# Performance work log

Hardware: AMD Instinct MI355X
Metric: run time of the kernel (lower is better)

Reference implementation:

```python
import jax, jax.numpy as jnp
import numpy as np

D = 1024; NH = 16; HD = 64; FF = 4096; DEPTH = 4
P = 14; C = 3; GRID = 32; MERGE = 2; NIMG = 4
L = GRID * GRID; S = NIMG * L; ORIG = 24; EPS = 1e-6
SCALE = HD ** -0.5


def setup_inputs() -> dict:
    key = jax.random.key(0)
    ks = jax.random.split(key, 12)
    s = 0.02
    return {
        "pixel_values": jax.random.normal(ks[0], (S, C * P * P), jnp.float32),
        "grid_thw": jnp.tile(jnp.array([[1, GRID, GRID]], jnp.int32), (NIMG, 1)),
        "conv_w": jax.random.normal(ks[1], (D, C * P * P), jnp.float32) * s,
        "conv_b": jnp.zeros((D,), jnp.float32),
        "pos_embed": jax.random.normal(ks[2], (ORIG * ORIG, D), jnp.float32) * s,
        "ln1_g": jnp.ones((DEPTH, D), jnp.float32),
        "ln1_b": jnp.zeros((DEPTH, D), jnp.float32),
        "qkv_w": jax.random.normal(ks[3], (DEPTH, 3 * D, D), jnp.float32) * s,
        "qkv_b": jnp.zeros((DEPTH, 3 * D), jnp.float32),
        "proj_w": jax.random.normal(ks[4], (DEPTH, D, D), jnp.float32) * s,
        "proj_b": jnp.zeros((DEPTH, D), jnp.float32),
        "ln2_g": jnp.ones((DEPTH, D), jnp.float32),
        "ln2_b": jnp.zeros((DEPTH, D), jnp.float32),
        "fc1_w": jax.random.normal(ks[5], (DEPTH, FF, D), jnp.float32) * s,
        "fc1_b": jnp.zeros((DEPTH, FF), jnp.float32),
        "fc2_w": jax.random.normal(ks[6], (DEPTH, D, FF), jnp.float32) * s,
        "fc2_b": jnp.zeros((DEPTH, D), jnp.float32),
    }


def _pos_ids():
    # rot_pos_emb spatial-merge permutation for one t=1 image, tiled over images
    h = jnp.broadcast_to(jnp.arange(GRID)[:, None], (GRID, GRID))
    w = jnp.broadcast_to(jnp.arange(GRID)[None, :], (GRID, GRID))
    def perm(a):
        a = a.reshape(GRID // MERGE, MERGE, GRID // MERGE, MERGE)
        return a.transpose(0, 2, 1, 3).reshape(-1)
    hpos = jnp.tile(perm(h), NIMG)  # [S]
    wpos = jnp.tile(perm(w), NIMG)
    return hpos, wpos


def _bilinear_border(img, nx, ny):
    # img [H, W, D]; nx, ny in [-1, 1]; align_corners=False, padding_mode='border'
    Hh, Ww, _ = img.shape
    x = (nx + 1.0) * 0.5 * Ww - 0.5
    y = (ny + 1.0) * 0.5 * Hh - 0.5
    x0 = jnp.floor(x); y0 = jnp.floor(y)
    wx = (x - x0)[:, None]; wy = (y - y0)[:, None]
    x0i = jnp.clip(x0.astype(jnp.int32), 0, Ww - 1)
    x1i = jnp.clip(x0.astype(jnp.int32) + 1, 0, Ww - 1)
    y0i = jnp.clip(y0.astype(jnp.int32), 0, Hh - 1)
    y1i = jnp.clip(y0.astype(jnp.int32) + 1, 0, Hh - 1)
    v00 = img[y0i, x0i]; v01 = img[y0i, x1i]
    v10 = img[y1i, x0i]; v11 = img[y1i, x1i]
    return (v00 * (1 - wy) * (1 - wx) + v01 * (1 - wy) * wx
            + v10 * wy * (1 - wx) + v11 * wy * wx)


def _ln(x, g, b):
    m = jnp.mean(x, axis=-1, keepdims=True)
    v = jnp.mean(jnp.square(x - m), axis=-1, keepdims=True)
    return (x - m) * jax.lax.rsqrt(v + EPS) * g + b


def _forward(pixel_values, conv_w, conv_b, pos_embed, ln1_g, ln1_b, qkv_w, qkv_b,
             proj_w, proj_b, ln2_g, ln2_b, fc1_w, fc1_b, fc2_w, fc2_b):
    # patch embed: conv with kernel==stride==patch over one patch == linear
    x = pixel_values @ conv_w.T + conv_b  # [S, D]

    # interpolated 2D position embedding (grid_sample bilinear, border pad)
    hpos, wpos = _pos_ids()
    norm_w = (wpos.astype(jnp.float32) + 0.5) / GRID * 2.0 - 1.0
    norm_h = (hpos.astype(jnp.float32) + 0.5) / GRID * 2.0 - 1.0
    pe = _bilinear_border(pos_embed.reshape(ORIG, ORIG, D), norm_w, norm_h)
    x = x + pe

    for i in range(DEPTH):
        # attention (block-diagonal over equal-length images -> batched)
        r = x
        y = _ln(x, ln1_g[i], ln1_b[i])
        qkv = (y @ qkv_w[i].T + qkv_b[i]).reshape(NIMG, L, 3, NH, HD)
        q = qkv[:, :, 0].transpose(0, 2, 1, 3)  # [B, H, L, hd]
        k = qkv[:, :, 1].transpose(0, 2, 1, 3)
        v = qkv[:, :, 2].transpose(0, 2, 1, 3)
        scores = jnp.einsum('bhqd,bhkd->bhqk', q, k) * SCALE
        probs = jax.nn.softmax(scores, axis=-1)
        o = jnp.einsum('bhqk,bhkd->bhqd', probs, v)
        o = o.transpose(0, 2, 1, 3).reshape(S, D)
        x = r + o @ proj_w[i].T + proj_b[i]
        # MLP
        r = x
        y = _ln(x, ln2_g[i], ln2_b[i])
        h = jax.nn.gelu(y @ fc1_w[i].T + fc1_b[i], approximate=False)
        x = r + h @ fc2_w[i].T + fc2_b[i]
    return x


def reference(pixel_values, grid_thw, conv_w, conv_b, pos_embed, ln1_g, ln1_b,
              qkv_w, qkv_b, proj_w, proj_b, ln2_g, ln2_b, fc1_w, fc1_b, fc2_w, fc2_b):
    return _forward(pixel_values, conv_w, conv_b, pos_embed, ln1_g, ln1_b, qkv_w,
                    qkv_b, proj_w, proj_b, ln2_g, ln2_b, fc1_w, fc1_b, fc2_w, fc2_b)
```

## Files before the change

kernel.cpp:

```cpp
#include <hip/hip_runtime.h>
#include <math.h>

typedef __bf16 bf16x8 __attribute__((ext_vector_type(8)));
typedef float f32x4 __attribute__((ext_vector_type(4)));
typedef short s16x4 __attribute__((ext_vector_type(4)));
typedef short s16x8 __attribute__((ext_vector_type(8)));

static __device__ __forceinline__ short f2bs(float f) {
  return __builtin_bit_cast(short, (__bf16)f);
}

#define GLL16(gp, lp) __builtin_amdgcn_global_load_lds( \
    (const __attribute__((address_space(1))) void*)(gp), \
    (__attribute__((address_space(3))) void*)(lp), 16, 0, 0)

__global__ __launch_bounds__(256) void cvt_f32_bf16(const float* __restrict__ s,
                                                    short* __restrict__ d, int n) {
  int stride = gridDim.x * blockDim.x * 4;
  for (int j = (blockIdx.x * blockDim.x + threadIdx.x) * 4; j < n; j += stride) {
    float4 v = *(const float4*)(s + j);
    s16x4 o;
    o[0] = f2bs(v.x); o[1] = f2bs(v.y); o[2] = f2bs(v.z); o[3] = f2bs(v.w);
    *(s16x4*)(d + j) = o;
  }
}

__global__ __launch_bounds__(256) void cvt_pad(const float* __restrict__ s,
                                               short* __restrict__ d) {
  int r = blockIdx.x;
  for (int c = threadIdx.x; c < 608; c += blockDim.x)
    d[(size_t)r * 608 + c] = (c < 588) ? f2bs(s[(size_t)r * 588 + c]) : (short)0;
}

template <int N, int K, int EPI, int CM, int CN>
__global__ __launch_bounds__(256) void gemm_bt(const short* __restrict__ A,
                                               const short* __restrict__ B,
                                               const float* __restrict__ bias,
                                               const float* __restrict__ resid,
                                               void* __restrict__ out) {
  static_assert(K % 32 == 0, "K");
  constexpr int NT = K / 32;
  static_assert(NT >= 3, "pipeline depth");
  constexpr int NX = N / 128, NY = 32;
  constexpr int nwg = NX * NY;
  static_assert(nwg % 8 == 0 && (nwg / 8) % (CM * CN) == 0, "chunk");
  static_assert(NX % CN == 0 && NY % CM == 0, "cells");
  __shared__ short lA[3][128 * 32];
  __shared__ short lB[3][128 * 32];

  const int o = blockIdx.x;
  const int wid = (o & 7) * (nwg / 8) + (o >> 3);
  constexpr int cellsz = CM * CN;
  const int cell = wid / cellsz, within = wid % cellsz;
  constexpr int cellsx = NX / CN;
  const int bm0 = ((cell / cellsx) * CM + within / CN) * 128;
  const int bn0 = ((cell % cellsx) * CN + within % CN) * 128;

  const int t = threadIdx.x, w = t >> 6, lane = t & 63;
  const int wr = w >> 1, wc = w & 1;
  f32x4 acc[4][4] = {};

  const int srow = t >> 2;
  const int scol = ((t & 3) ^ ((srow >> 1) & 3)) * 8;
  const short* aP = A + (size_t)(bm0 + srow) * K + scol;
  const short* bP = B + (size_t)(bn0 + srow) * K + scol;
  const int sdst0 = (w * 16) * 32;
  const int sdst1 = (64 + w * 16) * 32;

  const int lr = lane & 15;
  const int qx = ((lane >> 4) ^ ((lr >> 1) & 3)) * 8;

  auto stage = [&](int buf, int ko) {
    GLL16(aP + ko, &lA[buf][sdst0]);
    GLL16(aP + ko + (size_t)64 * K, &lA[buf][sdst1]);
    GLL16(bP + ko, &lB[buf][sdst0]);
    GLL16(bP + ko + (size_t)64 * K, &lB[buf][sdst1]);
  };

  stage(0, 0);
  stage(1, 32);
  stage(2, 64);

  int buf = 0;
  for (int kt = 0; kt < NT; ++kt) {
    if (kt < NT - 2)       asm volatile("s_waitcnt vmcnt(8)" ::: "memory");
    else if (kt == NT - 2) asm volatile("s_waitcnt vmcnt(4)" ::: "memory");
    else                   asm volatile("s_waitcnt vmcnt(0)" ::: "memory");
    __builtin_amdgcn_s_barrier();
    asm volatile("" ::: "memory");
    __builtin_amdgcn_sched_barrier(0);

    bf16x8 af[4], bg[4];
#pragma unroll
    for (int mi = 0; mi < 4; ++mi)
      af[mi] = *(const bf16x8*)&lA[buf][(wr * 64 + mi * 16 + lr) * 32 + qx];
#pragma unroll
    for (int ni = 0; ni < 4; ++ni)
      bg[ni] = *(const bf16x8*)&lB[buf][(wc * 64 + ni * 16 + lr) * 32 + qx];

    asm volatile("s_waitcnt lgkmcnt(0)" ::: "memory");
    __builtin_amdgcn_sched_barrier(0);
    __builtin_amdgcn_s_barrier();
    asm volatile("" ::: "memory");
    __builtin_amdgcn_sched_barrier(0);

    if (kt + 3 < NT) stage(buf, (kt + 3) * 32);
    __builtin_amdgcn_sched_barrier(0);

#pragma unroll
    for (int mi = 0; mi < 4; ++mi)
#pragma unroll
      for (int ni = 0; ni < 4; ++ni)
        acc[mi][ni] = __builtin_amdgcn_mfma_f32_16x16x32_bf16(af[mi], bg[ni],
                                                              acc[mi][ni], 0, 0, 0);
    buf = (buf == 2) ? 0 : buf + 1;
  }

  const int lg4 = (lane >> 4) * 4;
#pragma unroll
  for (int mi = 0; mi < 4; ++mi) {
#pragma unroll
    for (int ni = 0; ni < 4; ++ni) {
      const int row = bm0 + wr * 64 + mi * 16 + lg4;
      const int col = bn0 + wc * 64 + ni * 16 + lr;
      const float bc = bias[col];
#pragma unroll
      for (int r = 0; r < 4; ++r) {
        float v = acc[mi][ni][r] + bc;
        size_t idx = (size_t)(row + r) * N + col;
        if constexpr (EPI == 1) v = 0.5f * v * (1.0f + erff(v * 0.70710678118f));
        if constexpr (EPI == 0 || EPI == 1) ((short*)out)[idx] = f2bs(v);
        else if constexpr (EPI == 2) ((float*)out)[idx] = v + resid[idx];
        else ((float*)out)[idx] = v;
      }
    }
  }
}

template <int N, int KC, int LDK, int EPI, int CM, int CN, int KSPLIT>
__global__ __launch_bounds__(512, 2) void gemm256(const short* __restrict__ A,
                                                  const short* __restrict__ B,
                                                  const float* __restrict__ bias,
                                                  void* __restrict__ out) {
  static_assert(KC % 64 == 0, "K");
  constexpr int NKT = KC / 64;
  static_assert(NKT >= 3 && (NKT % 2) == 0, "ktiles");
  constexpr int NXT = N / 256, MYT = 16;
  constexpr int nwg = NXT * MYT * KSPLIT;
  constexpr int cellsz = CM * CN;
  static_assert(nwg % 8 == 0 && (nwg / 8) % cellsz == 0, "chunk");
  static_assert((NXT * MYT) % cellsz == 0, "cellspace");
  static_assert(NXT % CN == 0 && MYT % CM == 0, "cells");

  __shared__ short sA[2][2][8192];
  __shared__ short sB[2][2][8192];

  const int o = blockIdx.x;
  const int wid = (o & 7) * (nwg / 8) + (o >> 3);
  const int kc = wid / (NXT * MYT);
  const int rem = wid % (NXT * MYT);
  const int cell = rem / cellsz, within = rem % cellsz;
  constexpr int cellsx = NXT / CN;
  const int bm0 = ((cell / cellsx) * CM + within / CN) * 256;
  const int bn0 = ((cell % cellsx) * CN + within % CN) * 256;

  const int tid = threadIdx.x, wv = tid >> 6, lane = tid & 63;
  const int wrow = wv >> 2, wcol = wv & 3;
  const int lr = lane & 15, lg = lane >> 4;

  const int sr0 = tid >> 2;
  const int sc0 = ((tid & 3) ^ ((sr0 >> 1) & 3)) * 8;
  const short* aS0 = A + (size_t)(bm0 + sr0) * LDK + kc * KC + sc0;
  const short* bS0 = B + (size_t)(bn0 + sr0) * LDK + kc * KC + sc0;
  const int ld0 = wv * 512, ld1 = 4096 + wv * 512;

  auto stageA = [&](int d, int h, int kt) {
    const int off = kt * 64 + h * 32;
    GLL16(aS0 + off, &sA[d][h][ld0]);
    GLL16(aS0 + off + (size_t)128 * LDK, &sA[d][h][ld1]);
  };
  auto stageB = [&](int d, int h, int kt) {
    const int off = kt * 64 + h * 32;
    GLL16(bS0 + off, &sB[d][h][ld0]);
    GLL16(bS0 + off + (size_t)128 * LDK, &sB[d][h][ld1]);
  };

  const int chR = (lg ^ ((lr >> 1) & 3)) * 8;
  const int rA0 = wrow * 128 + lr;
  const int rB0 = wcol * 64 + lr;

  f32x4 acc[8][4] = {};

  stageA(0, 0, 0); stageB(0, 0, 0);
  stageA(0, 1, 0); stageB(0, 1, 0);
  stageA(1, 0, 1); stageB(1, 0, 1);
  asm volatile("s_waitcnt vmcnt(8)" ::: "memory");
  __builtin_amdgcn_sched_barrier(0);
  __builtin_amdgcn_s_barrier();

  bf16x8 af[4], bf[4];

#define LDA(mh, ks, d)                                                        \
  _Pragma("unroll")                                                           \
  for (int f = 0; f < 4; ++f)                                                 \
    af[f] = *(const bf16x8*)&sA[d][ks][(rA0 + (mh)*64 + f * 16) * 32 + chR];
#define LDB(ks, d)                                                            \
  _Pragma("unroll")                                                           \
  for (int n = 0; n < 4; ++n)                                                 \
    bf[n] = *(const bf16x8*)&sB[d][ks][(rB0 + n * 16) * 32 + chR];
#define MFMA16(mh)                                                            \
  __builtin_amdgcn_s_setprio(1);                                              \
  _Pragma("unroll")                                                           \
  for (int f = 0; f < 4; ++f)                                                 \
    _Pragma("unroll")                                                         \
    for (int n = 0; n < 4; ++n)                                               \
      acc[(mh)*4 + f][n] = __builtin_amdgcn_mfma_f32_16x16x32_bf16(           \
          af[f], bf[n], acc[(mh)*4 + f][n], 0, 0, 0);                         \
  __builtin_amdgcn_s_setprio(0);
#define PH_BAR1                                                               \
  __builtin_amdgcn_s_barrier();                                               \
  asm volatile("s_waitcnt lgkmcnt(0)" ::: "memory");                          \
  __builtin_amdgcn_sched_barrier(0);
#define PH_END                                                                \
  __builtin_amdgcn_s_barrier();
#define PH_END_V                                                              \
  asm volatile("s_waitcnt vmcnt(8)" ::: "memory");                            \
  __builtin_amdgcn_sched_barrier(0);                                          \
  __builtin_amdgcn_s_barrier();

  for (int t = 0; t < NKT; ++t) {
    const int d = t & 1;
    int t1 = t + 1; if (t1 >= NKT) t1 -= NKT;
    int t2 = t + 2; if (t2 >= NKT) t2 -= NKT;
    const int d1 = t1 & 1, d2 = t2 & 1;

    LDA(0, 0, d); LDB(0, d);
    stageA(d1, 1, t1);
    PH_BAR1; MFMA16(0); PH_END;
    LDA(1, 0, d);
    stageB(d1, 1, t1);
    PH_BAR1; MFMA16(1); PH_END_V;
    LDA(0, 1, d); LDB(1, d);
    stageA(d2, 0, t2);
    PH_BAR1; MFMA16(0); PH_END;
    LDA(1, 1, d);
    stageB(d2, 0, t2);
    PH_BAR1; MFMA16(1); PH_END_V;
  }
#undef LDA
#undef LDB
#undef MFMA16
#undef PH_BAR1
#undef PH_END
#undef PH_END_V

  const int lg4 = lg * 4;
#pragma unroll
  for (int mh = 0; mh < 2; ++mh) {
#pragma unroll
    for (int f = 0; f < 4; ++f) {
#pragma unroll
      for (int n = 0; n < 4; ++n) {
        const int row = bm0 + wrow * 128 + mh * 64 + f * 16 + lg4;
        const int col = bn0 + wcol * 64 + n * 16 + lr;
        float bc = 0.f;
        if constexpr (EPI != 5) bc = bias[col];
#pragma unroll
        for (int r = 0; r < 4; ++r) {
          float v = acc[mh * 4 + f][n][r] + bc;
          if constexpr (EPI == 1) v = 0.5f * v * (1.0f + erff(v * 0.70710678118f));
          if constexpr (EPI == 5)
            ((float*)out)[((size_t)kc << 22) + (size_t)(row + r) * N + col] = v;
          else
            ((short*)out)[(size_t)(row + r) * N + col] = f2bs(v);
        }
      }
    }
  }
}

__global__ __launch_bounds__(256) void fc2_reduce(const float* __restrict__ part,
                                                  const float* __restrict__ bias,
                                                  const float* __restrict__ resid,
                                                  float* __restrict__ dest) {
  const size_t i4 = ((size_t)blockIdx.x * 256 + threadIdx.x) * 4;
  const float4 a0 = *(const float4*)(part + i4);
  const float4 a1 = *(const float4*)(part + (1ull << 22) + i4);
  const float4 a2 = *(const float4*)(part + (2ull << 22) + i4);
  const float4 a3 = *(const float4*)(part + (3ull << 22) + i4);
  const float4 rv = *(const float4*)(resid + i4);
  const float4 bv = *(const float4*)(bias + (i4 & 1023));
  float4 o;
  o.x = a0.x + a1.x + a2.x + a3.x + rv.x + bv.x;
  o.y = a0.y + a1.y + a2.y + a3.y + rv.y + bv.y;
  o.z = a0.z + a1.z + a2.z + a3.z + rv.z + bv.z;
  o.w = a0.w + a1.w + a2.w + a3.w + rv.w + bv.w;
  *(float4*)(dest + i4) = o;
}

__global__ __launch_bounds__(256) void ln_fwd(const float* __restrict__ x,
                                              const float* __restrict__ g,
                                              const float* __restrict__ b,
                                              short* __restrict__ y) {
  const int row = blockIdx.x, t = threadIdx.x, w = t >> 6, lane = t & 63;
  const float4 v = ((const float4*)(x + (size_t)row * 1024))[t];
  float s = v.x + v.y + v.z + v.w;
  float ss = v.x * v.x + v.y * v.y + v.z * v.z + v.w * v.w;
#pragma unroll
  for (int m = 1; m < 64; m <<= 1) { s += __shfl_xor(s, m); ss += __shfl_xor(ss, m); }
  __shared__ float rs[4], rss[4];
  if (lane == 0) { rs[w] = s; rss[w] = ss; }
  __syncthreads();
  s = rs[0] + rs[1] + rs[2] + rs[3];
  ss = rss[0] + rss[1] + rss[2] + rss[3];
  const float mean = s * (1.f / 1024.f);
  const float var = ss * (1.f / 1024.f) - mean * mean;
  const float rstd = rsqrtf(var + 1e-6f);
  const float4 gv = ((const float4*)g)[t];
  const float4 bv = ((const float4*)b)[t];
  s16x4 o;
  o[0] = f2bs((v.x - mean) * rstd * gv.x + bv.x);
  o[1] = f2bs((v.y - mean) * rstd * gv.y + bv.y);
  o[2] = f2bs((v.z - mean) * rstd * gv.z + bv.z);
  o[3] = f2bs((v.w - mean) * rstd * gv.w + bv.w);
  *(s16x4*)(y + (size_t)row * 1024 + t * 4) = o;
}

__global__ __launch_bounds__(256) void pos_add(float* __restrict__ x,
                                               const float* __restrict__ pe) {
  const int sidx = blockIdx.x;
  const int f = sidx & 1023;
  const int wq = 2 * ((f >> 2) & 15) + (f & 1);
  const int hq = 2 * (f >> 6) + ((f >> 1) & 1);
  const float gx = (wq + 0.5f) * 0.75f - 0.5f;
  const float gy = (hq + 0.5f) * 0.75f - 0.5f;
  const float fx = floorf(gx), fy = floorf(gy);
  const float wx = gx - fx, wy = gy - fy;
  int x0 = (int)fx, y0 = (int)fy;
  const int x0i = x0 < 0 ? 0 : (x0 > 23 ? 23 : x0);
  const int x1i = (x0 + 1) < 0 ? 0 : ((x0 + 1) > 23 ? 23 : x0 + 1);
  const int y0i = y0 < 0 ? 0 : (y0 > 23 ? 23 : y0);
  const int y1i = (y0 + 1) < 0 ? 0 : ((y0 + 1) > 23 ? 23 : y0 + 1);
  const float w00 = (1 - wy) * (1 - wx), w01 = (1 - wy) * wx;
  const float w10 = wy * (1 - wx), w11 = wy * wx;
  const int c = threadIdx.x * 4;
  const float4 p00 = *(const float4*)(pe + (size_t)(y0i * 24 + x0i) * 1024 + c);
  const float4 p01 = *(const float4*)(pe + (size_t)(y0i * 24 + x1i) * 1024 + c);
  const float4 p10 = *(const float4*)(pe + (size_t)(y1i * 24 + x0i) * 1024 + c);
  const float4 p11 = *(const float4*)(pe + (size_t)(y1i * 24 + x1i) * 1024 + c);
  float* xp = x + (size_t)sidx * 1024 + c;
  float4 xv = *(float4*)xp;
  xv.x += w00 * p00.x + w01 * p01.x + w10 * p10.x + w11 * p11.x;
  xv.y += w00 * p00.y + w01 * p01.y + w10 * p10.y + w11 * p11.y;
  xv.z += w00 * p00.z + w01 * p01.z + w10 * p10.z + w11 * p11.z;
  xv.w += w00 * p00.w + w01 * p01.w + w10 * p10.w + w11 * p11.w;
  *(float4*)xp = xv;
}

__global__ __launch_bounds__(256) void attn_fwd(const short* __restrict__ qkv,
                                                short* __restrict__ outp) {
  __shared__ short lK[2][64 * 64];
  __shared__ short Vt[2][64 * 72];
  const int t = threadIdx.x, w = t >> 6, lane = t & 63;
  const int b = blockIdx.y >> 4, h = blockIdx.y & 15;
  const int sbase = b * 1024;
  const int q0 = blockIdx.x * 64 + w * 16;
  const int lr = lane & 15, lg = lane >> 4;

  const short* qrow = qkv + (size_t)(sbase + q0 + lr) * 3072 + h * 64;
  const bf16x8 qf0 = *(const bf16x8*)(qrow + lg * 8);
  const bf16x8 qf1 = *(const bf16x8*)(qrow + 32 + lg * 8);

  const int krofs = t >> 3;
  const int kcol = ((t & 7) ^ (krofs & 7)) * 8;
  const short* ksrc = qkv + (size_t)(sbase + krofs) * 3072 + 1024 + h * 64 + kcol;
  const int vkv = t >> 2, vdp = t & 3;
  const short* vsrc = qkv + (size_t)(sbase + vkv) * 3072 + 2048 + h * 64 + vdp * 16;
  const int vph = vkv ^ (vdp << 4);

  f32x4 o[4] = {};
  float mrun = -1e30f, lsum = 0.f;

  s16x8 v0 = *(const s16x8*)vsrc;
  s16x8 v1 = *(const s16x8*)(vsrc + 8);
  GLL16(ksrc, &lK[0][(w * 8) * 64]);
  GLL16(ksrc + (size_t)32 * 3072, &lK[0][(32 + w * 8) * 64]);
#pragma unroll
  for (int j = 0; j < 8; ++j) Vt[0][(vdp * 16 + j) * 72 + vph] = v0[j];
#pragma unroll
  for (int j = 0; j < 8; ++j) Vt[0][(vdp * 16 + 8 + j) * 72 + vph] = v1[j];
  asm volatile("s_waitcnt vmcnt(0) lgkmcnt(0)" ::: "memory");
  __builtin_amdgcn_s_barrier();

  int buf = 0;
  for (int kb = 0; kb < 16; ++kb) {
    if (kb < 15) {
      const short* vs = vsrc + (size_t)(kb + 1) * 64 * 3072;
      v0 = *(const s16x8*)vs;
      v1 = *(const s16x8*)(vs + 8);
      const short* ks = ksrc + (size_t)(kb + 1) * 64 * 3072;
      GLL16(ks, &lK[buf ^ 1][(w * 8) * 64]);
      GLL16(ks + (size_t)32 * 3072, &lK[buf ^ 1][(32 + w * 8) * 64]);
    }

    f32x4 s[4];
    __builtin_amdgcn_s_setprio(1);
#pragma unroll
    for (int sub = 0; sub < 4; ++sub) {
      const int krow = (sub * 16 + lr) * 64;
      const bf16x8 kf0 = *(const bf16x8*)&lK[buf][krow + (lg ^ (lr & 7)) * 8];
      const bf16x8 kf1 = *(const bf16x8*)&lK[buf][krow + ((lg + 4) ^ (lr & 7)) * 8];
      f32x4 a = {};
      a = __builtin_amdgcn_mfma_f32_16x16x32_bf16(kf0, qf0, a, 0, 0, 0);
      a = __builtin_amdgcn_mfma_f32_16x16x32_bf16(kf1, qf1, a, 0, 0, 0);
      s[sub] = a;
    }
    __builtin_amdgcn_s_setprio(0);

    constexpr float SC = 0.125f * 1.44269504089f;
    float sl[16];
#pragma unroll
    for (int sub = 0; sub < 4; ++sub)
#pragma unroll
      for (int r = 0; r < 4; ++r) sl[sub * 4 + r] = s[sub][r] * SC;
    float tm = sl[0];
#pragma unroll
    for (int i = 1; i < 16; ++i) tm = fmaxf(tm, sl[i]);
    tm = fmaxf(tm, __shfl_xor(tm, 16));
    tm = fmaxf(tm, __shfl_xor(tm, 32));
    if (!__all(tm <= mrun + 12.0f)) {
      const float newm = fmaxf(mrun, tm);
      const float sc = exp2f(mrun - newm);
      lsum *= sc;
#pragma unroll
      for (int f = 0; f < 4; ++f) {
        o[f][0] *= sc; o[f][1] *= sc; o[f][2] *= sc; o[f][3] *= sc;
      }
      mrun = newm;
    }
    s16x4 pb[4];
    float psum = 0.f;
#pragma unroll
    for (int sub = 0; sub < 4; ++sub)
#pragma unroll
      for (int r = 0; r < 4; ++r) {
        const float p = exp2f(sl[sub * 4 + r] - mrun);
        psum += p;
        pb[sub][r] = f2bs(p);
      }
    psum += __shfl_xor(psum, 16);
    psum += __shfl_xor(psum, 32);
    lsum += psum;

    __builtin_amdgcn_s_setprio(1);
#pragma unroll
    for (int f = 0; f < 4; ++f) {
      const int vrow = (f * 16 + lr) * 72;
#pragma unroll
      for (int sub = 0; sub < 4; ++sub) {
        const s16x4 va = *(const s16x4*)&Vt[buf][vrow + ((sub ^ f) << 4) + lg * 4];
        o[f] = __builtin_amdgcn_mfma_f32_16x16x16bf16_1k(va, pb[sub], o[f], 0, 0, 0);
      }
    }
    __builtin_amdgcn_s_setprio(0);

    if (kb < 15) {
#pragma unroll
      for (int j = 0; j < 8; ++j) Vt[buf ^ 1][(vdp * 16 + j) * 72 + vph] = v0[j];
#pragma unroll
      for (int j = 0; j < 8; ++j) Vt[buf ^ 1][(vdp * 16 + 8 + j) * 72 + vph] = v1[j];
      asm volatile("s_waitcnt vmcnt(0) lgkmcnt(0)" ::: "memory");
      __builtin_amdgcn_s_barrier();
      buf ^= 1;
    }
  }

  const float inv = 1.0f / lsum;
  short* orow = outp + (size_t)(sbase + q0 + lr) * 1024 + h * 64;
#pragma unroll
  for (int f = 0; f < 4; ++f) {
    s16x4 ov;
    ov[0] = f2bs(o[f][0] * inv); ov[1] = f2bs(o[f][1] * inv);
    ov[2] = f2bs(o[f][2] * inv); ov[3] = f2bs(o[f][3] * inv);
    *(s16x4*)(orow + f * 16 + lg * 4) = ov;
  }
}

extern "C" void kernel_launch(void* const* d_in, const int* in_sizes, int n_in,
                              void* d_out, int out_size, void* d_ws, size_t ws_size,
                              hipStream_t stream) {
  const float* pixel  = (const float*)d_in[0];
  const float* conv_w = (const float*)d_in[2];
  const float* conv_b = (const float*)d_in[3];
  const float* pos_e  = (const float*)d_in[4];
  const float* ln1_g  = (const float*)d_in[5];
  const float* ln1_b  = (const float*)d_in[6];
  const float* qkv_w  = (const float*)d_in[7];
  const float* qkv_b  = (const float*)d_in[8];
  const float* proj_w = (const float*)d_in[9];
  const float* proj_b = (const float*)d_in[10];
  const float* ln2_g  = (const float*)d_in[11];
  const float* ln2_b  = (const float*)d_in[12];
  const float* fc1_w  = (const float*)d_in[13];
  const float* fc1_b  = (const float*)d_in[14];
  const float* fc2_w  = (const float*)d_in[15];
  const float* fc2_b  = (const float*)d_in[16];

  char* ws = (char*)d_ws;
  short* wQKV  = (short*)(ws + 0);
  short* wPROJ = (short*)(ws + 25165824);
  short* wFC1  = (short*)(ws + 33554432);
  short* wFC2  = (short*)(ws + 67108864);
  float* X     = (float*)(ws + 100663296);
  short* Y     = (short*)(ws + 117440512);
  short* QKVB  = (short*)(ws + 125829120);
  short* ATTNO = (short*)(ws + 150994944);
  short* H     = QKVB;
  short* WPIX  = QKVB;
  short* WCONV = (short*)(ws + 125829120 + 4980736);
  float* PART  = (float*)(ws + 159383552);
  const bool wsbig = ws_size >= (size_t)159383552 + 67108864;

  cvt_f32_bf16<<<2048, 256, 0, stream>>>(qkv_w, wQKV, 4 * 3072 * 1024);
  cvt_f32_bf16<<<1024, 256, 0, stream>>>(proj_w, wPROJ, 4 * 1024 * 1024);
  cvt_f32_bf16<<<2048, 256, 0, stream>>>(fc1_w, wFC1, 4 * 4096 * 1024);
  cvt_f32_bf16<<<2048, 256, 0, stream>>>(fc2_w, wFC2, 4 * 1024 * 4096);
  cvt_pad<<<4096, 256, 0, stream>>>(pixel, WPIX);
  cvt_pad<<<1024, 256, 0, stream>>>(conv_w, WCONV);

  gemm_bt<1024, 608, 3, 4, 8><<<256, 256, 0, stream>>>(WPIX, WCONV, conv_b, nullptr, X);
  pos_add<<<4096, 256, 0, stream>>>(X, pos_e);

  for (int i = 0; i < 4; ++i) {
    ln_fwd<<<4096, 256, 0, stream>>>(X, ln1_g + i * 1024, ln1_b + i * 1024, Y);
    gemm256<3072, 1024, 1024, 0, 8, 3, 1><<<192, 512, 0, stream>>>(
        Y, wQKV + (size_t)i * 3072 * 1024, qkv_b + i * 3072, QKVB);
    attn_fwd<<<dim3(16, 64), 256, 0, stream>>>(QKVB, ATTNO);
    gemm_bt<1024, 1024, 2, 4, 8><<<256, 256, 0, stream>>>(
        ATTNO, wPROJ + (size_t)i * 1024 * 1024, proj_b + i * 1024, X, X);
    ln_fwd<<<4096, 256, 0, stream>>>(X, ln2_g + i * 1024, ln2_b + i * 1024, Y);
    gemm256<4096, 1024, 1024, 1, 8, 4, 1><<<256, 512, 0, stream>>>(
        Y, wFC1 + (size_t)i * 4096 * 1024, fc1_b + i * 4096, H);
    float* dest = (i < 3) ? X : (float*)d_out;
    if (wsbig) {
      gemm256<1024, 1024, 4096, 5, 8, 4, 4><<<256, 512, 0, stream>>>(
          H, wFC2 + (size_t)i * 1024 * 4096, nullptr, PART);
      fc2_reduce<<<4096, 256, 0, stream>>>(PART, fc2_b + i * 1024, X, dest);
    } else {
      gemm_bt<1024, 4096, 2, 4, 8><<<256, 256, 0, stream>>>(
          H, wFC2 + (size_t)i * 1024 * 4096, fc2_b + i * 1024, X, dest);
    }
  }
}
```

Measured before the change: 1.022 ms.

## Restructure gemm256 main loop into two-barrier phases with full A/B fragment loads

Replaces the four-phase-per-k-tile schedule, which had four barrier pairs and split A/B staging, with a phase macro. Each phase loads both A halves and the B fragments, issues the stageA and stageB for a future half-tile together, then runs 32 MFMAs behind a single barrier pair. The loop is unrolled by two k-tiles and the prefetch indices are adjusted. This roughly halves the barriers and waitcnt stalls per tile, at the cost of more live fragment registers, larger MFMA bursts and a stricter NKT>=4 requirement.

```diff
diff --git a/kernel.cpp b/kernel.cpp
--- a/kernel.cpp
+++ b/kernel.cpp
@@ -144,7 +144,7 @@
                                                   void* __restrict__ out) {
   static_assert(KC % 64 == 0, "K");
   constexpr int NKT = KC / 64;
-  static_assert(NKT >= 3 && (NKT % 2) == 0, "ktiles");
+  static_assert(NKT >= 4 && (NKT % 2) == 0, "ktiles");
   constexpr int NXT = N / 256, MYT = 16;
   constexpr int nwg = NXT * MYT * KSPLIT;
   constexpr int cellsz = CM * CN;
@@ -190,6 +190,7 @@
   const int rB0 = wcol * 64 + lr;
 
   f32x4 acc[8][4] = {};
+  bf16x8 a0[4], a1[4], bb[4];
 
   stageA(0, 0, 0); stageB(0, 0, 0);
   stageA(0, 1, 0); stageB(0, 1, 0);
@@ -198,61 +199,49 @@
   __builtin_amdgcn_sched_barrier(0);
   __builtin_amdgcn_s_barrier();
 
-  bf16x8 af[4], bf[4];
-
-#define LDA(mh, ks, d)                                                        \
-  _Pragma("unroll")                                                           \
-  for (int f = 0; f < 4; ++f)                                                 \
-    af[f] = *(const bf16x8*)&sA[d][ks][(rA0 + (mh)*64 + f * 16) * 32 + chR];
-#define LDB(ks, d)                                                            \
-  _Pragma("unroll")                                                           \
-  for (int n = 0; n < 4; ++n)                                                 \
-    bf[n] = *(const bf16x8*)&sB[d][ks][(rB0 + n * 16) * 32 + chR];
-#define MFMA16(mh)                                                            \
-  __builtin_amdgcn_s_setprio(1);                                              \
-  _Pragma("unroll")                                                           \
-  for (int f = 0; f < 4; ++f)                                                 \
+#define PHASE(ks, dd, sd, sh, skt)                                            \
+  {                                                                           \
+    _Pragma("unroll")                                                         \
+    for (int f = 0; f < 4; ++f)                                               \
+      a0[f] = *(const bf16x8*)&sA[dd][ks][(rA0 + f * 16) * 32 + chR];         \
+    _Pragma("unroll")                                                         \
+    for (int f = 0; f < 4; ++f)                                               \
+      a1[f] = *(const bf16x8*)&sA[dd][ks][(rA0 + 64 + f * 16) * 32 + chR];    \
     _Pragma("unroll")                                                         \
     for (int n = 0; n < 4; ++n)                                               \
-      acc[(mh)*4 + f][n] = __builtin_amdgcn_mfma_f32_16x16x32_bf16(           \
-          af[f], bf[n], acc[(mh)*4 + f][n], 0, 0, 0);                         \
-  __builtin_amdgcn_s_setprio(0);
-#define PH_BAR1                                                               \
-  __builtin_amdgcn_s_barrier();                                               \
-  asm volatile("s_waitcnt lgkmcnt(0)" ::: "memory");                          \
-  __builtin_amdgcn_sched_barrier(0);
-#define PH_END                                                                \
-  __builtin_amdgcn_s_barrier();
-#define PH_END_V                                                              \
-  asm volatile("s_waitcnt vmcnt(8)" ::: "memory");                            \
-  __builtin_amdgcn_sched_barrier(0);                                          \
-  __builtin_amdgcn_s_barrier();
-
-  for (int t = 0; t < NKT; ++t) {
-    const int d = t & 1;
-    int t1 = t + 1; if (t1 >= NKT) t1 -= NKT;
-    int t2 = t + 2; if (t2 >= NKT) t2 -= NKT;
-    const int d1 = t1 & 1, d2 = t2 & 1;
-
-    LDA(0, 0, d); LDB(0, d);
-    stageA(d1, 1, t1);
-    PH_BAR1; MFMA16(0); PH_END;
-    LDA(1, 0, d);
-    stageB(d1, 1, t1);
-    PH_BAR1; MFMA16(1); PH_END_V;
-    LDA(0, 1, d); LDB(1, d);
-    stageA(d2, 0, t2);
-    PH_BAR1; MFMA16(0); PH_END;
-    LDA(1, 1, d);
-    stageB(d2, 0, t2);
-    PH_BAR1; MFMA16(1); PH_END_V;
-  }
-#undef LDA
-#undef LDB
-#undef MFMA16
-#undef PH_BAR1
-#undef PH_END
-#undef PH_END_V
+      bb[n] = *(const bf16x8*)&sB[dd][ks][(rB0 + n * 16) * 32 + chR];         \
+    stageA(sd, sh, skt);                                                      \
+    stageB(sd, sh, skt);                                                      \
+    __builtin_amdgcn_s_barrier();                                             \
+    asm volatile("s_waitcnt lgkmcnt(0)" ::: "memory");                        \
+    __builtin_amdgcn_sched_barrier(0);                                        \
+    __builtin_amdgcn_s_setprio(1);                                            \
+    _Pragma("unroll")                                                         \
+    for (int f = 0; f < 4; ++f)                                               \
+      _Pragma("unroll")                                                       \
+      for (int n = 0; n < 4; ++n)                                             \
+        acc[f][n] = __builtin_amdgcn_mfma_f32_16x16x32_bf16(                  \
+            a0[f], bb[n], acc[f][n], 0, 0, 0);                                \
+    _Pragma("unroll")                                                         \
+    for (int f = 0; f < 4; ++f)                                               \
+      _Pragma("unroll")                                                       \
+      for (int n = 0; n < 4; ++n)                                             \
+        acc[4 + f][n] = __builtin_amdgcn_mfma_f32_16x16x32_bf16(              \
+            a1[f], bb[n], acc[4 + f][n], 0, 0, 0);                            \
+    __builtin_amdgcn_s_setprio(0);                                            \
+    asm volatile("s_waitcnt vmcnt(8)" ::: "memory");                          \
+    __builtin_amdgcn_s_barrier();                                             \
+  }
+
+  for (int tt = 0; tt < NKT; tt += 2) {
+    int u2 = tt + 2; if (u2 >= NKT) u2 -= NKT;
+    int u3 = tt + 3; if (u3 >= NKT) u3 -= NKT;
+    PHASE(0, 0, 1, 1, tt + 1);
+    PHASE(1, 0, 0, 0, u2);
+    PHASE(0, 1, 0, 1, u2);
+    PHASE(1, 1, 1, 0, u3);
+  }
+#undef PHASE
 
   const int lg4 = lg * 4;
 #pragma unroll
```

After: 1.001 ms. 2.1% less time.
